# Kernel optimization log

Measured on AMD Instinct MI355X. Metric: run time of the kernel, lower is better.

The kernel has to match this reference:

```python
import jax, jax.numpy as jnp
import numpy as np

N_EMBED = 2048
NUM_EXPERTS = 64
TOP_K = 8
B, S = 4, 4096


def setup_inputs() -> dict:
    key = jax.random.key(0)
    k_x, k_n, k_w1, k_b1, k_w2, k_b2 = jax.random.split(key, 6)
    bound = 1.0 / np.sqrt(N_EMBED)  # torch nn.Linear default init range
    return {
        "x": jax.random.normal(k_x, (B, S, N_EMBED), dtype=jnp.float32),
        "noise": jax.random.normal(k_n, (B, S, NUM_EXPERTS), dtype=jnp.float32),
        "W1": jax.random.uniform(k_w1, (N_EMBED, NUM_EXPERTS), jnp.float32, -bound, bound),
        "b1": jax.random.uniform(k_b1, (NUM_EXPERTS,), jnp.float32, -bound, bound),
        "W2": jax.random.uniform(k_w2, (N_EMBED, NUM_EXPERTS), jnp.float32, -bound, bound),
        "b2": jax.random.uniform(k_b2, (NUM_EXPERTS,), jnp.float32, -bound, bound),
    }


def reference(x, noise, W1, b1, W2, b2):
    # logits = lin1(x); noise_scale = softplus(lin2(x))
    logits = jnp.einsum("bsd,de->bse", x, W1) + b1          # [B,S,E]
    scale = jax.nn.softplus(jnp.einsum("bsd,de->bse", x, W2) + b2)
    mixed = logits + noise * scale                            # [B,S,E]
    full = jax.nn.softmax(mixed, axis=-1)

    topk_vals, topk_idx = jax.lax.top_k(mixed, TOP_K)         # [B,S,K]

    # scatter topk values into a -inf background, then softmax (masked softmax)
    E = mixed.shape[-1]
    flat_mixed = mixed.reshape(-1, E)
    flat_idx = topk_idx.reshape(-1, TOP_K)
    flat_vals = topk_vals.reshape(-1, TOP_K)
    rows = jnp.arange(flat_mixed.shape[0])[:, None]
    sparse = jnp.full_like(flat_mixed, -jnp.inf).at[rows, flat_idx].set(flat_vals)
    sparse_sm = jax.nn.softmax(sparse, axis=-1).reshape(mixed.shape)

    return sparse_sm, topk_idx, full
```

## Files before the change

### kernel.cpp

```cpp
#include <hip/hip_runtime.h>
#include <math.h>


typedef _Float16 f16x8 __attribute__((ext_vector_type(8)));
typedef _Float16 f16x4 __attribute__((ext_vector_type(4)));
typedef float f32x4 __attribute__((ext_vector_type(4)));

constexpr int ND = 2048, NE = 64, NK = 8, NTOK = 16384;
constexpr int KC   = 32;
constexpr int NCHT = ND / KC;
constexpr int CPSG = 4;
constexpr int NSTG = NCHT / CPSG;
constexpr int HSTG = NSTG / 2;
constexpr int MTOK = 16;
constexpr int ZROW = 132;
constexpr int STG_F16 = CPSG * MTOK * 64;

__global__ void prep_w(const float* __restrict__ W1, const float* __restrict__ W2,
                       _Float16* __restrict__ wt3) {
    const int g    = blockIdx.x * 256 + threadIdx.x;
    const int cg   = g >> 9;
    const int rem  = g & 511;
    const int t    = rem >> 6;
    const int lane = rem & 63;
    const int col  = lane & 15, q = lane >> 4;
    const int n    = t * 16 + col;
    const float* W = (t < 4) ? W1 : W2;
    const int cn   = n & 63;
    _Float16 h[8], l[8];
    #pragma unroll
    for (int j = 0; j < 8; ++j) {
        const float v = W[(size_t)(cg * 32 + q * 8 + j) * 64 + cn];
        const _Float16 hh = (_Float16)v;
        h[j] = hh;
        l[j] = (_Float16)((v - (float)hh) * 2048.0f);
    }
    *(f16x8*)&wt3[((size_t)(cg * 2 + 0) * 8 + t) * 512 + lane * 8] = *(f16x8*)h;
    *(f16x8*)&wt3[((size_t)(cg * 2 + 1) * 8 + t) * 512 + lane * 8] = *(f16x8*)l;
}

__device__ __forceinline__ void split4(const float4 v, f16x4& hh, f16x4& ll) {
    const _Float16 h0 = (_Float16)v.x, h1 = (_Float16)v.y,
                   h2 = (_Float16)v.z, h3 = (_Float16)v.w;
    hh = (f16x4){h0, h1, h2, h3};
    ll = (f16x4){(_Float16)((v.x - (float)h0) * 2048.0f),
                 (_Float16)((v.y - (float)h1) * 2048.0f),
                 (_Float16)((v.z - (float)h2) * 2048.0f),
                 (_Float16)((v.w - (float)h3) * 2048.0f)};
}

__device__ __forceinline__ void block_sync_lds() {
    asm volatile("s_waitcnt lgkmcnt(0)" ::: "memory");
    __builtin_amdgcn_s_barrier();
}

__global__ __launch_bounds__(256, 4)
void router_fused(const float* __restrict__ x, const _Float16* __restrict__ wt3,
                  const float* __restrict__ noise,
                  const float* __restrict__ b1, const float* __restrict__ b2,
                  float* __restrict__ out_sparse, float* __restrict__ out_idx,
                  float* __restrict__ out_full) {
    __shared__ __align__(16) _Float16 stage[2][STG_F16];
    const int tid  = threadIdx.x;
    const int lane = tid & 63;
    const int wu   = __builtin_amdgcn_readfirstlane(tid >> 6);
    const int col  = lane & 15, q = lane >> 4;
    const long tok0 = (long)blockIdx.x * MTOK;
    const int ta = 2 * wu, tb = 2 * wu + 1;

    const int stok = tid >> 4, fsub = tid & 15;
    const float* xs = x + (tok0 + stok) * (size_t)ND + fsub * 4;
    const int g8 = fsub & 7;
    const int wS = g8 >> 1, wh = g8 & 1;

    const _Float16* wla = wt3 + (size_t)ta * 512 + (size_t)lane * 8;
    const _Float16* wlb = wt3 + (size_t)tb * 512 + (size_t)lane * 8;

    f32x4 a0[2], a1[2], zk0[2];
    #pragma unroll
    for (int i = 0; i < 2; ++i)
        #pragma unroll
        for (int r = 0; r < 4; ++r) { a0[i][r] = 0.f; a1[i][r] = 0.f; }

    auto loadX = [&](float4 (&xr)[2], const int s) {
        #pragma unroll
        for (int j = 0; j < 2; ++j)
            xr[j] = *(const float4*)(xs + (size_t)s * 128 + (size_t)j * 64);
    };
    auto deposit = [&](_Float16* wb, const float4 (&xr)[2]) {
        #pragma unroll
        for (int j = 0; j < 2; ++j) {
            const int cc = j * 2 + (fsub >> 3);
            f16x4 hv, lv; split4(xr[j], hv, lv);
            const int idx = ((cc * MTOK + stok) << 6)
                          + (((wS ^ (stok & 7) ^ ((cc & 1) << 2)) << 3) + (wh << 2));
            *(f16x4*)&wb[idx]      = hv;
            *(f16x4*)&wb[idx ^ 32] = lv;
        }
    };

    auto do_stage = [&](const int s, const _Float16* rb, _Float16* wb) {
        f16x8 B[CPSG][4];
        #pragma unroll
        for (int cc = 0; cc < 2; ++cc) {
            const size_t cb = (size_t)(s * CPSG + cc) * 8192;
            B[cc][0] = *(const f16x8*)(wla + cb);
            B[cc][1] = *(const f16x8*)(wlb + cb);
            B[cc][2] = *(const f16x8*)(wla + cb + 4096);
            B[cc][3] = *(const f16x8*)(wlb + cb + 4096);
        }
        #pragma unroll
        for (int cc = 2; cc < CPSG; ++cc) {
            const size_t cb = (size_t)(s * CPSG + cc) * 8192;
            B[cc][0] = *(const f16x8*)(wla + cb);
            B[cc][1] = *(const f16x8*)(wlb + cb);
            B[cc][2] = *(const f16x8*)(wla + cb + 4096);
            B[cc][3] = *(const f16x8*)(wlb + cb + 4096);
        }
        float4 xl[2];
        if (s + 1 < NSTG) loadX(xl, s + 1);
        #pragma unroll
        for (int cc = 0; cc < CPSG; ++cc) {
            const int swz = (cc & 1) << 2;
            const int ridx = ((cc * MTOK + col) << 6)
                           + ((q ^ (col & 7) ^ swz) << 3);
            const f16x8 ah = *(const f16x8*)&rb[ridx];
            const f16x8 al = *(const f16x8*)&rb[ridx ^ 32];
            a0[0] = __builtin_amdgcn_mfma_f32_16x16x32_f16(ah, B[cc][0], a0[0], 0, 0, 0);
            a0[1] = __builtin_amdgcn_mfma_f32_16x16x32_f16(ah, B[cc][1], a0[1], 0, 0, 0);
            a1[0] = __builtin_amdgcn_mfma_f32_16x16x32_f16(ah, B[cc][2], a1[0], 0, 0, 0);
            a1[1] = __builtin_amdgcn_mfma_f32_16x16x32_f16(ah, B[cc][3], a1[1], 0, 0, 0);
            a1[0] = __builtin_amdgcn_mfma_f32_16x16x32_f16(al, B[cc][0], a1[0], 0, 0, 0);
            a1[1] = __builtin_amdgcn_mfma_f32_16x16x32_f16(al, B[cc][1], a1[1], 0, 0, 0);
        }
        if (s == HSTG - 1) {
            #pragma unroll
            for (int i = 0; i < 2; ++i) {
                zk0[i] = a0[i] + a1[i] * 4.8828125e-4f;
                #pragma unroll
                for (int r = 0; r < 4; ++r) { a0[i][r] = 0.f; a1[i][r] = 0.f; }
            }
        }
        if (s + 1 < NSTG) deposit(wb, xl);
        block_sync_lds();
    };

    {
        float4 x0[2];
        loadX(x0, 0);
        deposit(stage[0], x0);
    }
    block_sync_lds();

    for (int sp = 0; sp < NSTG; sp += 2) {
        do_stage(sp,     stage[0], stage[1]);
        do_stage(sp + 1, stage[1], stage[0]);
    }

    float* zs = (float*)&stage[0][0];
    #pragma unroll
    for (int i = 0; i < 2; ++i) {
        const int n = (ta + i) * 16 + col;
        #pragma unroll
        for (int r = 0; r < 4; ++r) {
            const float zk1 = a0[i][r] + a1[i][r] * 4.8828125e-4f;
            const float comb = (float)((double)zk0[i][r] + (double)zk1);
            zs[(q * 4 + r) * ZROW + n] = comb;
        }
    }
    __syncthreads();

    const float b1v = b1[lane];
    const float b2v = b2[lane];
    for (int tt = 0; tt < 4; ++tt) {
        const int lt = wu * 4 + tt;
        const long tok = tok0 + lt;
        const float z1 = zs[lt * ZROW + lane] + b1v;
        const float z2 = zs[lt * ZROW + 64 + lane] + b2v;
        const float sc = (float)log1p(exp((double)z2));
        const float nz = noise[tok * NE + lane];
        const float mixed = z1 + nz * sc;

        float vmax = mixed;
        for (int off = 32; off; off >>= 1) vmax = fmaxf(vmax, __shfl_xor(vmax, off));
        const float e = expf(mixed - vmax);
        float denom = e;
        for (int off = 32; off; off >>= 1) denom += __shfl_xor(denom, off);
        const float fullv = e / denom;

        float cur = mixed;
        int   sel = 0;
        float myidxf = 0.0f;
        #pragma unroll
        for (int r = 0; r < NK; ++r) {
            float bv = cur; int bi = lane;
            for (int off = 32; off; off >>= 1) {
                const float ov = __shfl_xor(bv, off);
                const int   oi = __shfl_xor(bi, off);
                if (ov > bv || (ov == bv && oi < bi)) { bv = ov; bi = oi; }
            }
            if (lane == r)  myidxf = (float)bi;
            if (lane == bi) { sel = 1; cur = -INFINITY; }
        }

        const float es = sel ? e : 0.0f;
        float dsum = es;
        for (int off = 32; off; off >>= 1) dsum += __shfl_xor(dsum, off);
        const float sparsev = sel ? (e / dsum) : 0.0f;

        out_full[tok * NE + lane]   = fullv;
        out_sparse[tok * NE + lane] = sparsev;
        if (lane < NK) out_idx[tok * NK + lane] = myidxf;
    }
}

extern "C" void kernel_launch(void* const* d_in, const int* in_sizes, int n_in,
                              void* d_out, int out_size, void* d_ws, size_t ws_size,
                              hipStream_t stream) {
    const float* x     = (const float*)d_in[0];
    const float* noise = (const float*)d_in[1];
    const float* W1    = (const float*)d_in[2];
    const float* b1    = (const float*)d_in[3];
    const float* W2    = (const float*)d_in[4];
    const float* b2    = (const float*)d_in[5];

    float* out_sparse = (float*)d_out;
    float* out_idx    = out_sparse + (size_t)NTOK * NE;
    float* out_full   = out_idx + (size_t)NTOK * NK;

    _Float16* wt3 = (_Float16*)d_ws;

    prep_w<<<128, 256, 0, stream>>>(W1, W2, wt3);
    router_fused<<<NTOK / MTOK, 256, 0, stream>>>(x, wt3, noise, b1, b2,
                                                  out_sparse, out_idx, out_full);
}
```

Baseline: 249.6 us.

## Split the K dimension across two blocks with a last-arriver combine

Each 16-token group is now handled by two blocks, each reducing half of the 2048-wide embedding. Each block writes its partial logits to a workspace slot and increments an atomic per-group counter, and the second block to arrive combines both halves and runs the softmax/top-k epilogue. The counters are zeroed in prep_w, and launch bounds rise from 4 to 6 blocks per CU. The aim is more blocks and higher occupancy to hide memory latency, at the cost of a global round-trip for the partials, atomics and fences, plus extra register pressure from the tighter launch bound.

```diff
diff --git a/kernel.cpp b/kernel.cpp
--- a/kernel.cpp
+++ b/kernel.cpp
@@ -8,16 +8,18 @@
 
 constexpr int ND = 2048, NE = 64, NK = 8, NTOK = 16384;
 constexpr int KC   = 32;
-constexpr int NCHT = ND / KC;
 constexpr int CPSG = 4;
-constexpr int NSTG = NCHT / CPSG;
-constexpr int HSTG = NSTG / 2;
+constexpr int NSTG = 8;
 constexpr int MTOK = 16;
+constexpr int NGRP = NTOK / MTOK;
 constexpr int ZROW = 132;
 constexpr int STG_F16 = CPSG * MTOK * 64;
 
 __global__ void prep_w(const float* __restrict__ W1, const float* __restrict__ W2,
-                       _Float16* __restrict__ wt3) {
+                       _Float16* __restrict__ wt3, int* __restrict__ flags) {
+    if (blockIdx.x == 0) {
+        for (int t = threadIdx.x; t < NGRP; t += 256) flags[t] = 0;
+    }
     const int g    = blockIdx.x * 256 + threadIdx.x;
     const int cg   = g >> 9;
     const int rem  = g & 511;
@@ -54,29 +56,33 @@
     __builtin_amdgcn_s_barrier();
 }
 
-__global__ __launch_bounds__(256, 4)
+__global__ __launch_bounds__(256, 6)
 void router_fused(const float* __restrict__ x, const _Float16* __restrict__ wt3,
                   const float* __restrict__ noise,
                   const float* __restrict__ b1, const float* __restrict__ b2,
+                  float* __restrict__ zpart, int* __restrict__ flags,
                   float* __restrict__ out_sparse, float* __restrict__ out_idx,
                   float* __restrict__ out_full) {
     __shared__ __align__(16) _Float16 stage[2][STG_F16];
+    __shared__ int sflag;
     const int tid  = threadIdx.x;
     const int lane = tid & 63;
     const int wu   = __builtin_amdgcn_readfirstlane(tid >> 6);
     const int col  = lane & 15, q = lane >> 4;
-    const long tok0 = (long)blockIdx.x * MTOK;
+    const int grp  = blockIdx.x >> 1;
+    const int ks   = blockIdx.x & 1;
+    const long tok0 = (long)grp * MTOK;
     const int ta = 2 * wu, tb = 2 * wu + 1;
 
     const int stok = tid >> 4, fsub = tid & 15;
-    const float* xs = x + (tok0 + stok) * (size_t)ND + fsub * 4;
+    const float* xs = x + (tok0 + stok) * (size_t)ND + (size_t)ks * 1024 + fsub * 4;
     const int g8 = fsub & 7;
     const int wS = g8 >> 1, wh = g8 & 1;
 
     const _Float16* wla = wt3 + (size_t)ta * 512 + (size_t)lane * 8;
     const _Float16* wlb = wt3 + (size_t)tb * 512 + (size_t)lane * 8;
 
-    f32x4 a0[2], a1[2], zk0[2];
+    f32x4 a0[2], a1[2];
     #pragma unroll
     for (int i = 0; i < 2; ++i)
         #pragma unroll
@@ -102,16 +108,8 @@
     auto do_stage = [&](const int s, const _Float16* rb, _Float16* wb) {
         f16x8 B[CPSG][4];
         #pragma unroll
-        for (int cc = 0; cc < 2; ++cc) {
-            const size_t cb = (size_t)(s * CPSG + cc) * 8192;
-            B[cc][0] = *(const f16x8*)(wla + cb);
-            B[cc][1] = *(const f16x8*)(wlb + cb);
-            B[cc][2] = *(const f16x8*)(wla + cb + 4096);
-            B[cc][3] = *(const f16x8*)(wlb + cb + 4096);
-        }
-        #pragma unroll
-        for (int cc = 2; cc < CPSG; ++cc) {
-            const size_t cb = (size_t)(s * CPSG + cc) * 8192;
+        for (int cc = 0; cc < CPSG; ++cc) {
+            const size_t cb = (size_t)((ks * 32 + s * CPSG + cc)) * 8192;
             B[cc][0] = *(const f16x8*)(wla + cb);
             B[cc][1] = *(const f16x8*)(wlb + cb);
             B[cc][2] = *(const f16x8*)(wla + cb + 4096);
@@ -133,14 +131,6 @@
             a1[0] = __builtin_amdgcn_mfma_f32_16x16x32_f16(al, B[cc][0], a1[0], 0, 0, 0);
             a1[1] = __builtin_amdgcn_mfma_f32_16x16x32_f16(al, B[cc][1], a1[1], 0, 0, 0);
         }
-        if (s == HSTG - 1) {
-            #pragma unroll
-            for (int i = 0; i < 2; ++i) {
-                zk0[i] = a0[i] + a1[i] * 4.8828125e-4f;
-                #pragma unroll
-                for (int r = 0; r < 4; ++r) { a0[i][r] = 0.f; a1[i][r] = 0.f; }
-            }
-        }
         if (s + 1 < NSTG) deposit(wb, xl);
         block_sync_lds();
     };
@@ -157,14 +147,35 @@
         do_stage(sp + 1, stage[1], stage[0]);
     }
 
-    float* zs = (float*)&stage[0][0];
+    f32x4 zk[2];
+    #pragma unroll
+    for (int i = 0; i < 2; ++i)
+        zk[i] = a0[i] + a1[i] * 4.8828125e-4f;
+
+    float* myslot = zpart + ((size_t)(grp * 2 + ks)) * (MTOK * 128);
     #pragma unroll
     for (int i = 0; i < 2; ++i) {
         const int n = (ta + i) * 16 + col;
         #pragma unroll
+        for (int r = 0; r < 4; ++r)
+            myslot[(q * 4 + r) * 128 + n] = zk[i][r];
+    }
+    __threadfence();
+    __syncthreads();
+    if (tid == 0) sflag = atomicAdd(&flags[grp], 1);
+    __syncthreads();
+    if (sflag == 0) return;
+    __threadfence();
+
+    const float* pslot = zpart + ((size_t)(grp * 2 + (1 - ks))) * (MTOK * 128);
+    float* zs = (float*)&stage[0][0];
+    #pragma unroll
+    for (int i = 0; i < 2; ++i) {
+        const int n = (ta + i) * 16 + col;
+        #pragma unroll
         for (int r = 0; r < 4; ++r) {
-            const float zk1 = a0[i][r] + a1[i][r] * 4.8828125e-4f;
-            const float comb = (float)((double)zk0[i][r] + (double)zk1);
+            const float pv = pslot[(q * 4 + r) * 128 + n];
+            const float comb = (float)((double)zk[i][r] + (double)pv);
             zs[(q * 4 + r) * ZROW + n] = comb;
         }
     }
@@ -228,9 +239,12 @@
     float* out_idx    = out_sparse + (size_t)NTOK * NE;
     float* out_full   = out_idx + (size_t)NTOK * NK;
 
-    _Float16* wt3 = (_Float16*)d_ws;
-
-    prep_w<<<128, 256, 0, stream>>>(W1, W2, wt3);
-    router_fused<<<NTOK / MTOK, 256, 0, stream>>>(x, wt3, noise, b1, b2,
-                                                  out_sparse, out_idx, out_full);
-}
+    float*    zpart = (float*)d_ws;
+    _Float16* wt3   = (_Float16*)((char*)d_ws + ((size_t)16 << 20));
+    int*      flags = (int*)((char*)d_ws + ((size_t)17 << 20));
+
+    prep_w<<<128, 256, 0, stream>>>(W1, W2, wt3, flags);
+    router_fused<<<NGRP * 2, 256, 0, stream>>>(x, wt3, noise, b1, b2,
+                                               zpart, flags,
+                                               out_sparse, out_idx, out_full);
+}
```

New measurement: 957.9 us. 284% more time.
